# Performance work log

Measured on AMD Instinct MI355X. Metric: run time of the kernel, lower is better.

The kernel has to match this reference:

```python
import jax, jax.numpy as jnp
import numpy as np

B, C, H, W = 8, 64, 64, 64
MID = C // 8  # = 8, single-head key/query dim


def setup_inputs() -> dict:
    key = jax.random.key(0)
    ks = jax.random.split(key, 8)
    return {
        "x": jax.random.normal(ks[0], (B, C, H, W), dtype=jnp.float32),
        "wq": jax.random.normal(ks[1], (MID, C), dtype=jnp.float32) * 0.1,
        "bq": jax.random.normal(ks[2], (MID,), dtype=jnp.float32) * 0.1,
        "wk": jax.random.normal(ks[3], (MID, C), dtype=jnp.float32) * 0.1,
        "bk": jax.random.normal(ks[4], (MID,), dtype=jnp.float32) * 0.1,
        "wv": jax.random.normal(ks[5], (C, C), dtype=jnp.float32) * 0.1,
        "bv": jax.random.normal(ks[6], (C,), dtype=jnp.float32) * 0.1,
        "gamma": jax.random.uniform(ks[7], (1,), dtype=jnp.float32),
    }


def reference(x, wq, bq, wk, bk, wv, bv, gamma):
    b, c, h, w = x.shape
    n = h * w
    xf = x.reshape(b, c, n)  # [B, C, N]
    # 1x1 convs == per-pixel linear projections
    q = jnp.einsum("mc,bcn->bmn", wq, xf) + bq[:, None]  # [B, MID, N]
    k = jnp.einsum("mc,bcn->bmn", wk, xf) + bk[:, None]  # [B, MID, N]
    v = jnp.einsum("dc,bcn->bdn", wv, xf) + bv[:, None]  # [B, C, N]
    # attn[b, i, j] = softmax_j( q[:, i] . k[:, j] )  -- no scaling (SAGAN)
    attn = jax.nn.softmax(jnp.einsum("bmi,bmj->bij", q, k), axis=-1)  # [B, N, N]
    # out[b, c, i] = sum_j v[b, c, j] * attn[b, i, j]
    out = jnp.einsum("bcj,bij->bci", v, attn).reshape(b, c, h, w)
    return x + gamma[0] * out
```

## Files before the change

### kernel.cpp

```cpp
#include <hip/hip_runtime.h>
#include <math.h>

#define NB 8
#define NC 64
#define NN 4096
#define SHIFTC 20.0f

typedef __attribute__((ext_vector_type(8))) short short8;
typedef __attribute__((ext_vector_type(4))) float float4v;
typedef __attribute__((ext_vector_type(4))) unsigned int uint4v;
typedef __attribute__((ext_vector_type(2))) int int2v;

__device__ inline unsigned short f2bf(float f) {
    unsigned int u = __builtin_bit_cast(unsigned int, f);
    unsigned int r = (u + 0x7FFFu + ((u >> 16) & 1u)) >> 16;
    return (unsigned short)r;
}
__device__ inline unsigned int bfpack(float lo, float hi) {
    unsigned int a = __builtin_bit_cast(unsigned int, lo) + 0x8000u;
    unsigned int b = __builtin_bit_cast(unsigned int, hi) + 0x8000u;
    return __builtin_amdgcn_perm(b, a, 0x07060302u);
}
__device__ inline unsigned int cvtpk(float lo, float hi) {
    unsigned int r;
    asm("v_cvt_pk_bf16_f32 %0, %1, %2" : "=v"(r) : "v"(lo), "v"(hi));
    return r;
}
__device__ inline void plswap(unsigned int& x, unsigned int& y) {
    int2v r = __builtin_amdgcn_permlane32_swap((int)x, (int)y, false, false);
    x = (unsigned int)r[0];
    y = (unsigned int)r[1];
}

__global__ __launch_bounds__(256) void proj_mfma_kernel(
    const float* __restrict__ x,
    const float* __restrict__ wq, const float* __restrict__ bq,
    const float* __restrict__ wk, const float* __restrict__ bk,
    const float* __restrict__ wv, const float* __restrict__ bv,
    unsigned short* __restrict__ qo8, unsigned short* __restrict__ ko8,
    unsigned short* __restrict__ vo)
{
    const int b = blockIdx.y;
    const int wave = threadIdx.x >> 6, lane = threadIdx.x & 63;
    const int c0 = lane & 15, quad = lane >> 4;
    const int n0 = blockIdx.x * 64 + wave * 16;

    __shared__ unsigned short qkb[4][16][24];

    const float* xb = x + (size_t)b * NC * NN + n0 + c0;
    short8 xf[2];
#pragma unroll
    for (int kc = 0; kc < 2; ++kc)
#pragma unroll
        for (int e = 0; e < 8; ++e)
            xf[kc][e] = (short)f2bf(xb[(size_t)(kc * 32 + quad * 8 + e) * NN]);

    const int c0p = (c0 & 3) | ((c0 & 8) >> 1) | ((c0 & 4) << 1);

#pragma unroll
    for (int mt = 0; mt < 4; ++mt) {
        short8 wf0, wf1;
#pragma unroll
        for (int e = 0; e < 8; ++e) {
            wf0[e] = (short)f2bf(wv[(mt * 16 + c0) * 64 + quad * 8 + e]);
            wf1[e] = (short)f2bf(wv[(mt * 16 + c0) * 64 + 32 + quad * 8 + e]);
        }
        float4v acc = {0.f, 0.f, 0.f, 0.f};
        acc = __builtin_amdgcn_mfma_f32_16x16x32_bf16(wf0, xf[0], acc, 0, 0, 0);
        acc = __builtin_amdgcn_mfma_f32_16x16x32_bf16(wf1, xf[1], acc, 0, 0, 0);
#pragma unroll
        for (int reg = 0; reg < 4; ++reg) {
            int ch = mt * 16 + quad * 4 + reg;
            vo[((size_t)b * NC + ch) * NN + n0 + c0p] = f2bf(acc[reg] + bv[ch]);
        }
    }

    {
        const float* wrow = (c0 < 8) ? (wq + c0 * 64) : (wk + (c0 - 8) * 64);
        short8 wf0, wf1;
#pragma unroll
        for (int e = 0; e < 8; ++e) {
            wf0[e] = (short)f2bf(wrow[quad * 8 + e]);
            wf1[e] = (short)f2bf(wrow[32 + quad * 8 + e]);
        }
        float4v acc = {0.f, 0.f, 0.f, 0.f};
        acc = __builtin_amdgcn_mfma_f32_16x16x32_bf16(wf0, xf[0], acc, 0, 0, 0);
        acc = __builtin_amdgcn_mfma_f32_16x16x32_bf16(wf1, xf[1], acc, 0, 0, 0);
        float a[4];
#pragma unroll
        for (int reg = 0; reg < 4; ++reg) {
            int qr = quad * 4 + reg;
            float bias = (qr < 8) ? bq[qr] : bk[qr - 8];
            a[reg] = acc[reg] + bias;
        }
        *(uint2*)&qkb[wave][c0][quad * 4] = make_uint2(bfpack(a[0], a[1]), bfpack(a[2], a[3]));
        if (quad == 0) {
            uint4 qrow = *(const uint4*)&qkb[wave][c0][0];
            uint4 krow = *(const uint4*)&qkb[wave][c0][8];
            *(uint4*)&qo8[((size_t)b * NN + n0 + c0) * 8] = qrow;
            *(uint4*)&ko8[((size_t)b * NN + n0 + c0) * 8] = krow;
        }
    }
}

__global__ __launch_bounds__(256, 4) void attn_fused_kernel(
    const unsigned short* __restrict__ qo8, const unsigned short* __restrict__ ko8,
    const unsigned short* __restrict__ vo,
    const float* __restrict__ x, const float* __restrict__ gamma,
    float* __restrict__ out)
{
    const int b = blockIdx.y;
    const int i0b = blockIdx.x * 32;
    const int wave = threadIdx.x >> 6, lane = threadIdx.x & 63;
    const int c0 = lane & 15, quad = lane >> 4;

    __shared__ __align__(16) float oacc[32][65];
    __shared__ float lbuf[4][2][16];

    for (int i = threadIdx.x; i < 32 * 65; i += 256)
        ((float*)oacc)[i] = 0.f;
    __syncthreads();

    const int jbase = wave * (NN / 4);

    short8 qf[2] = {};
    if (quad == 0) {
        qf[0] = *(const short8*)(qo8 + ((size_t)b * NN + i0b + c0) * 8);
        qf[1] = *(const short8*)(qo8 + ((size_t)b * NN + i0b + 16 + c0) * 8);
    }

    float4v acc[2][4];
#pragma unroll
    for (int qh = 0; qh < 2; ++qh)
#pragma unroll
        for (int ct = 0; ct < 4; ++ct) acc[qh][ct] = (float4v){0.f, 0.f, 0.f, 0.f};
    float lsum[2] = {0.f, 0.f};

    const unsigned short* vbase = vo + ((size_t)b * NC + c0) * NN + jbase + quad * 8;
    const unsigned short* kbase = ko8 + ((size_t)(b * NN + jbase + c0)) * 8;

    for (int t = 0; t < NN / 4 / 64; ++t) {
        const int jt = t * 64;
        short8 kf[4] = {};
        if (quad == 0) {
#pragma unroll
            for (int st = 0; st < 4; ++st)
                kf[st] = *(const short8*)(kbase + (size_t)(jt + st * 16) * 8);
        }
        short8 vf[4][2];
#pragma unroll
        for (int ct = 0; ct < 4; ++ct)
#pragma unroll
            for (int kc = 0; kc < 2; ++kc)
                vf[ct][kc] = *(const short8*)(vbase + (size_t)ct * 16 * NN + jt + kc * 32);

#pragma unroll
        for (int qh = 0; qh < 2; ++qh) {
            const float4v mC = {-SHIFTC, -SHIFTC, -SHIFTC, -SHIFTC};
            float4v s[4];
#pragma unroll
            for (int st = 0; st < 4; ++st)
                s[st] = __builtin_amdgcn_mfma_f32_16x16x32_bf16(kf[st], qf[qh], mC, 0, 0, 0);

            unsigned int D[4][2];
            float ls = 0.f;
#pragma unroll
            for (int st = 0; st < 4; ++st) {
                float p0 = __expf(s[st][0]);
                float p1 = __expf(s[st][1]);
                float p2 = __expf(s[st][2]);
                float p3 = __expf(s[st][3]);
                ls += (p0 + p1) + (p2 + p3);
                D[st][0] = cvtpk(p0, p1);
                D[st][1] = cvtpk(p2, p3);
            }
            lsum[qh] += ls;

            unsigned int a00 = D[0][0], b00 = D[1][0];  plswap(a00, b00);
            unsigned int a01 = D[0][1], b01 = D[1][1];  plswap(a01, b01);
            unsigned int a10 = D[2][0], b10 = D[3][0];  plswap(a10, b10);
            unsigned int a11 = D[2][1], b11 = D[3][1];  plswap(a11, b11);
            uint4v u0 = {a00, a01, b00, b01};
            uint4v u1 = {a10, a11, b10, b11};
            short8 pf0 = __builtin_bit_cast(short8, u0);
            short8 pf1 = __builtin_bit_cast(short8, u1);

#pragma unroll
            for (int ct = 0; ct < 4; ++ct)
                acc[qh][ct] = __builtin_amdgcn_mfma_f32_16x16x32_bf16(
                    pf0, vf[ct][0], acc[qh][ct], 0, 0, 0);
#pragma unroll
            for (int ct = 0; ct < 4; ++ct)
                acc[qh][ct] = __builtin_amdgcn_mfma_f32_16x16x32_bf16(
                    pf1, vf[ct][1], acc[qh][ct], 0, 0, 0);
        }
    }

#pragma unroll
    for (int qh = 0; qh < 2; ++qh) {
        lsum[qh] += __shfl_xor(lsum[qh], 16);
        lsum[qh] += __shfl_xor(lsum[qh], 32);
    }
    if (quad == 0) {
        lbuf[wave][0][c0] = lsum[0];
        lbuf[wave][1][c0] = lsum[1];
    }

#pragma unroll
    for (int qh = 0; qh < 2; ++qh)
#pragma unroll
        for (int ct = 0; ct < 4; ++ct)
#pragma unroll
            for (int reg = 0; reg < 4; ++reg)
                atomicAdd(&oacc[qh * 16 + quad * 4 + reg][ct * 16 + c0], acc[qh][ct][reg]);
    __syncthreads();

    const int q = threadIdx.x & 31;
    const int cg = threadIdx.x >> 5;
    const float L = lbuf[0][q >> 4][q & 15] + lbuf[1][q >> 4][q & 15] +
                    lbuf[2][q >> 4][q & 15] + lbuf[3][q >> 4][q & 15];
    const float scale = gamma[0] / L;
    const size_t base = (size_t)b * NC * NN + i0b + q;
#pragma unroll
    for (int cc = 0; cc < 8; ++cc) {
        const int ch = cg * 8 + cc;
        const float O = oacc[q][ch];
        const size_t idx = base + (size_t)ch * NN;
        out[idx] = x[idx] + scale * O;
    }
}

extern "C" void kernel_launch(void* const* d_in, const int* in_sizes, int n_in,
                              void* d_out, int out_size, void* d_ws, size_t ws_size,
                              hipStream_t stream) {
    const float* x     = (const float*)d_in[0];
    const float* wq    = (const float*)d_in[1];
    const float* bq    = (const float*)d_in[2];
    const float* wk    = (const float*)d_in[3];
    const float* bk    = (const float*)d_in[4];
    const float* wv    = (const float*)d_in[5];
    const float* bv    = (const float*)d_in[6];
    const float* gamma = (const float*)d_in[7];
    float* out = (float*)d_out;

    unsigned short* wss = (unsigned short*)d_ws;
    unsigned short* qo8 = wss;
    unsigned short* ko8 = qo8 + (size_t)NB * NN * 8;
    unsigned short* vo  = ko8 + (size_t)NB * NN * 8;

    proj_mfma_kernel<<<dim3(NN / 64, NB), 256, 0, stream>>>(
        x, wq, bq, wk, bk, wv, bv, qo8, ko8, vo);
    attn_fused_kernel<<<dim3(NN / 32, NB), 256, 0, stream>>>(
        qo8, ko8, vo, x, gamma, out);
}
```

Before: 163.2 us.

## Halve query tile per block to 16 rows and use bfpack conversion

The attention kernel now handles 16 query rows per block instead of 32, which doubles the grid and halves the register accumulators and LDS per block. K and V tiles are now reused across only one query half, so global/L2 traffic for K/V roughly doubles in exchange for more parallelism and lower register pressure. The packed bf16 conversion of probabilities switches from the hardware cvt_pk instruction to a manual round-and-permute helper.

```diff
diff --git a/kernel.cpp b/kernel.cpp
--- a/kernel.cpp
+++ b/kernel.cpp
@@ -20,11 +20,6 @@
     unsigned int a = __builtin_bit_cast(unsigned int, lo) + 0x8000u;
     unsigned int b = __builtin_bit_cast(unsigned int, hi) + 0x8000u;
     return __builtin_amdgcn_perm(b, a, 0x07060302u);
-}
-__device__ inline unsigned int cvtpk(float lo, float hi) {
-    unsigned int r;
-    asm("v_cvt_pk_bf16_f32 %0, %1, %2" : "=v"(r) : "v"(lo), "v"(hi));
-    return r;
 }
 __device__ inline void plswap(unsigned int& x, unsigned int& y) {
     int2v r = __builtin_amdgcn_permlane32_swap((int)x, (int)y, false, false);
@@ -110,31 +105,27 @@
     float* __restrict__ out)
 {
     const int b = blockIdx.y;
-    const int i0b = blockIdx.x * 32;
+    const int i0b = blockIdx.x * 16;
     const int wave = threadIdx.x >> 6, lane = threadIdx.x & 63;
     const int c0 = lane & 15, quad = lane >> 4;
 
-    __shared__ __align__(16) float oacc[32][65];
-    __shared__ float lbuf[4][2][16];
-
-    for (int i = threadIdx.x; i < 32 * 65; i += 256)
+    __shared__ __align__(16) float oacc[16][65];
+    __shared__ float lbuf[4][16];
+
+    for (int i = threadIdx.x; i < 16 * 65; i += 256)
         ((float*)oacc)[i] = 0.f;
     __syncthreads();
 
     const int jbase = wave * (NN / 4);
 
-    short8 qf[2] = {};
-    if (quad == 0) {
-        qf[0] = *(const short8*)(qo8 + ((size_t)b * NN + i0b + c0) * 8);
-        qf[1] = *(const short8*)(qo8 + ((size_t)b * NN + i0b + 16 + c0) * 8);
-    }
-
-    float4v acc[2][4];
-#pragma unroll
-    for (int qh = 0; qh < 2; ++qh)
-#pragma unroll
-        for (int ct = 0; ct < 4; ++ct) acc[qh][ct] = (float4v){0.f, 0.f, 0.f, 0.f};
-    float lsum[2] = {0.f, 0.f};
+    short8 qf = {};
+    if (quad == 0)
+        qf = *(const short8*)(qo8 + ((size_t)b * NN + i0b + c0) * 8);
+
+    float4v acc[4];
+#pragma unroll
+    for (int ct = 0; ct < 4; ++ct) acc[ct] = (float4v){0.f, 0.f, 0.f, 0.f};
+    float lsum = 0.f;
 
     const unsigned short* vbase = vo + ((size_t)b * NC + c0) * NN + jbase + quad * 8;
     const unsigned short* kbase = ko8 + ((size_t)(b * NN + jbase + c0)) * 8;
@@ -154,76 +145,65 @@
             for (int kc = 0; kc < 2; ++kc)
                 vf[ct][kc] = *(const short8*)(vbase + (size_t)ct * 16 * NN + jt + kc * 32);
 
-#pragma unroll
-        for (int qh = 0; qh < 2; ++qh) {
-            const float4v mC = {-SHIFTC, -SHIFTC, -SHIFTC, -SHIFTC};
-            float4v s[4];
-#pragma unroll
-            for (int st = 0; st < 4; ++st)
-                s[st] = __builtin_amdgcn_mfma_f32_16x16x32_bf16(kf[st], qf[qh], mC, 0, 0, 0);
-
-            unsigned int D[4][2];
-            float ls = 0.f;
-#pragma unroll
-            for (int st = 0; st < 4; ++st) {
-                float p0 = __expf(s[st][0]);
-                float p1 = __expf(s[st][1]);
-                float p2 = __expf(s[st][2]);
-                float p3 = __expf(s[st][3]);
-                ls += (p0 + p1) + (p2 + p3);
-                D[st][0] = cvtpk(p0, p1);
-                D[st][1] = cvtpk(p2, p3);
-            }
-            lsum[qh] += ls;
-
-            unsigned int a00 = D[0][0], b00 = D[1][0];  plswap(a00, b00);
-            unsigned int a01 = D[0][1], b01 = D[1][1];  plswap(a01, b01);
-            unsigned int a10 = D[2][0], b10 = D[3][0];  plswap(a10, b10);
-            unsigned int a11 = D[2][1], b11 = D[3][1];  plswap(a11, b11);
-            uint4v u0 = {a00, a01, b00, b01};
-            uint4v u1 = {a10, a11, b10, b11};
-            short8 pf0 = __builtin_bit_cast(short8, u0);
-            short8 pf1 = __builtin_bit_cast(short8, u1);
-
-#pragma unroll
-            for (int ct = 0; ct < 4; ++ct)
-                acc[qh][ct] = __builtin_amdgcn_mfma_f32_16x16x32_bf16(
-                    pf0, vf[ct][0], acc[qh][ct], 0, 0, 0);
-#pragma unroll
-            for (int ct = 0; ct < 4; ++ct)
-                acc[qh][ct] = __builtin_amdgcn_mfma_f32_16x16x32_bf16(
-                    pf1, vf[ct][1], acc[qh][ct], 0, 0, 0);
-        }
-    }
-
-#pragma unroll
-    for (int qh = 0; qh < 2; ++qh) {
-        lsum[qh] += __shfl_xor(lsum[qh], 16);
-        lsum[qh] += __shfl_xor(lsum[qh], 32);
-    }
-    if (quad == 0) {
-        lbuf[wave][0][c0] = lsum[0];
-        lbuf[wave][1][c0] = lsum[1];
-    }
-
-#pragma unroll
-    for (int qh = 0; qh < 2; ++qh)
+        const float4v mC = {-SHIFTC, -SHIFTC, -SHIFTC, -SHIFTC};
+        float4v s[4];
+#pragma unroll
+        for (int st = 0; st < 4; ++st)
+            s[st] = __builtin_amdgcn_mfma_f32_16x16x32_bf16(kf[st], qf, mC, 0, 0, 0);
+
+        unsigned int D[4][2];
+        float ls = 0.f;
+#pragma unroll
+        for (int st = 0; st < 4; ++st) {
+            float p0 = __expf(s[st][0]);
+            float p1 = __expf(s[st][1]);
+            float p2 = __expf(s[st][2]);
+            float p3 = __expf(s[st][3]);
+            ls += (p0 + p1) + (p2 + p3);
+            D[st][0] = bfpack(p0, p1);
+            D[st][1] = bfpack(p2, p3);
+        }
+        lsum += ls;
+
+        unsigned int a00 = D[0][0], b00 = D[1][0];  plswap(a00, b00);
+        unsigned int a01 = D[0][1], b01 = D[1][1];  plswap(a01, b01);
+        unsigned int a10 = D[2][0], b10 = D[3][0];  plswap(a10, b10);
+        unsigned int a11 = D[2][1], b11 = D[3][1];  plswap(a11, b11);
+        uint4v u0 = {a00, a01, b00, b01};
+        uint4v u1 = {a10, a11, b10, b11};
+        short8 pf0 = __builtin_bit_cast(short8, u0);
+        short8 pf1 = __builtin_bit_cast(short8, u1);
+
 #pragma unroll
         for (int ct = 0; ct < 4; ++ct)
-#pragma unroll
-            for (int reg = 0; reg < 4; ++reg)
-                atomicAdd(&oacc[qh * 16 + quad * 4 + reg][ct * 16 + c0], acc[qh][ct][reg]);
+            acc[ct] = __builtin_amdgcn_mfma_f32_16x16x32_bf16(
+                pf0, vf[ct][0], acc[ct], 0, 0, 0);
+#pragma unroll
+        for (int ct = 0; ct < 4; ++ct)
+            acc[ct] = __builtin_amdgcn_mfma_f32_16x16x32_bf16(
+                pf1, vf[ct][1], acc[ct], 0, 0, 0);
+    }
+
+    lsum += __shfl_xor(lsum, 16);
+    lsum += __shfl_xor(lsum, 32);
+    if (quad == 0)
+        lbuf[wave][c0] = lsum;
+
+#pragma unroll
+    for (int ct = 0; ct < 4; ++ct)
+#pragma unroll
+        for (int reg = 0; reg < 4; ++reg)
+            atomicAdd(&oacc[quad * 4 + reg][ct * 16 + c0], acc[ct][reg]);
     __syncthreads();
 
-    const int q = threadIdx.x & 31;
-    const int cg = threadIdx.x >> 5;
-    const float L = lbuf[0][q >> 4][q & 15] + lbuf[1][q >> 4][q & 15] +
-                    lbuf[2][q >> 4][q & 15] + lbuf[3][q >> 4][q & 15];
+    const int q = threadIdx.x & 15;
+    const int cg = threadIdx.x >> 4;
+    const float L = lbuf[0][q] + lbuf[1][q] + lbuf[2][q] + lbuf[3][q];
     const float scale = gamma[0] / L;
     const size_t base = (size_t)b * NC * NN + i0b + q;
 #pragma unroll
-    for (int cc = 0; cc < 8; ++cc) {
-        const int ch = cg * 8 + cc;
+    for (int cc = 0; cc < 4; ++cc) {
+        const int ch = cg * 4 + cc;
         const float O = oacc[q][ch];
         const size_t idx = base + (size_t)ch * NN;
         out[idx] = x[idx] + scale * O;
@@ -250,6 +230,6 @@
 
     proj_mfma_kernel<<<dim3(NN / 64, NB), 256, 0, stream>>>(
         x, wq, bq, wk, bk, wv, bv, qo8, ko8, vo);
-    attn_fused_kernel<<<dim3(NN / 32, NB), 256, 0, stream>>>(
+    attn_fused_kernel<<<dim3(NN / 16, NB), 256, 0, stream>>>(
         qo8, ko8, vo, x, gamma, out);
 }
```

After: 284.7 us. 1.74x slower.
